# Performance work log

Hardware: AMD Instinct MI355X
Metric: run time of the kernel (lower is better)

Reference implementation:

```python
import jax, jax.numpy as jnp
import numpy as np

N, E, H, HEADS, L, B = 16000, 256000, 192, 4, 4, 8
C = H // HEADS
VN, VE, T = 32, 8, 1000


def _sin_emb(t, dim):
    half = dim // 2
    freqs = jnp.exp(-np.log(10000.0) * jnp.arange(half, dtype=jnp.float32) / half)
    ang = t.astype(jnp.float32)[:, None] * freqs[None, :]
    return jnp.concatenate([jnp.sin(ang), jnp.cos(ang)], axis=-1)


def _ln(x, g, b, eps=1e-5):
    mu = jnp.mean(x, -1, keepdims=True)
    var = jnp.mean(jnp.square(x - mu), -1, keepdims=True)
    return (x - mu) * jax.lax.rsqrt(var + eps) * g + b


def setup_inputs():
    key = jax.random.key(0)
    ks = iter(jax.random.split(key, 64))
    p = lambda shape, s=0.02: jax.random.normal(next(ks), shape, jnp.float32) * s
    inp = {}
    inp['node_emb'] = p((VN, H))
    inp['edge_emb'] = p((VE, H))
    inp['time_w1'] = p((H, H)); inp['time_b1'] = jnp.zeros((H,), jnp.float32)
    inp['time_w2'] = p((H, H)); inp['time_b2'] = jnp.zeros((H,), jnp.float32)
    inp['mask_emb'] = p((2, H))
    inp['wq'] = p((L, H, H)); inp['bq'] = jnp.zeros((L, H), jnp.float32)
    inp['wk'] = p((L, H, H)); inp['bk'] = jnp.zeros((L, H), jnp.float32)
    inp['wv'] = p((L, H, H)); inp['bv'] = jnp.zeros((L, H), jnp.float32)
    inp['we'] = p((L, H, H))
    inp['wskip'] = p((L, H, H)); inp['bskip'] = jnp.zeros((L, H), jnp.float32)
    inp['wbeta'] = p((L, 3 * H))
    inp['ln_g'] = jnp.ones((L, H), jnp.float32); inp['ln_b'] = jnp.zeros((L, H), jnp.float32)
    inp['node_out_w'] = p((H, VN)); inp['node_out_b'] = jnp.zeros((VN,), jnp.float32)
    inp['edge_w1'] = p((4 * H, H)); inp['edge_b1'] = jnp.zeros((H,), jnp.float32)
    inp['edge_w2'] = p((H, VE)); inp['edge_b2'] = jnp.zeros((VE,), jnp.float32)
    inp['node_type'] = jax.random.randint(next(ks), (N,), 0, VN)
    inp['edge_type'] = jax.random.randint(next(ks), (E,), 0, VE)
    inp['edge_index'] = jax.random.randint(next(ks), (2, E), 0, N)
    inp['edit_mask'] = jax.random.randint(next(ks), (N,), 0, 2, dtype=jnp.int32)
    inp['node_batch'] = jnp.sort(jax.random.randint(next(ks), (N,), 0, B))
    inp['t_graph'] = jax.random.randint(next(ks), (B,), 1, T)
    return inp


def reference(node_emb, edge_emb, time_w1, time_b1, time_w2, time_b2, mask_emb,
              wq, bq, wk, bk, wv, bv, we, wskip, bskip, wbeta, ln_g, ln_b,
              node_out_w, node_out_b, edge_w1, edge_b1, edge_w2, edge_b2,
              node_type, edge_type, edge_index, edit_mask, node_batch, t_graph):
    src, dst = edge_index[0], edge_index[1]
    # time embedding: sinusoidal -> Linear -> SiLU -> Linear  => [B, H]
    t_vec = jax.nn.silu(_sin_emb(t_graph, H) @ time_w1 + time_b1) @ time_w2 + time_b2
    t_node = t_vec[node_batch]              # [N, H]
    t_edge = t_vec[node_batch[src]]         # [E, H]
    x = node_emb[node_type] + t_node + mask_emb[edit_mask]
    edge_attr = edge_emb[edge_type] + t_edge
    scale = 1.0 / np.sqrt(C)
    for l in range(L):
        q = (x @ wq[l] + bq[l]).reshape(N, HEADS, C)
        k = (x @ wk[l] + bk[l]).reshape(N, HEADS, C)
        v = (x @ wv[l] + bv[l]).reshape(N, HEADS, C)
        e = (edge_attr @ we[l]).reshape(E, HEADS, C)
        kj = k[src] + e                                   # [E, heads, C]
        score = jnp.sum(q[dst] * kj, axis=-1) * scale      # [E, heads]
        m = jax.ops.segment_max(score, dst, num_segments=N)
        ex = jnp.exp(score - m[dst])
        denom = jax.ops.segment_sum(ex, dst, num_segments=N)
        alpha = ex / denom[dst]
        msg = (v[src] + e) * alpha[..., None]              # [E, heads, C]
        out = jax.ops.segment_sum(msg, dst, num_segments=N).reshape(N, H)
        xr = x @ wskip[l] + bskip[l]
        beta = jax.nn.sigmoid(jnp.concatenate([out, xr, out - xr], -1) @ wbeta[l])[:, None]
        h = beta * xr + (1.0 - beta) * out
        x = _ln(x + h, ln_g[l], ln_b[l])
    node_logits = x @ node_out_w + node_out_b
    edge_feat = jnp.concatenate([x[src], x[dst], edge_attr, t_edge], -1)  # [E, 4H]
    edge_logits = jax.nn.silu(edge_feat @ edge_w1 + edge_b1) @ edge_w2 + edge_b2
    return node_logits, edge_logits
```

## Files before the change

### kernel.cpp

```cpp
#include <hip/hip_runtime.h>
#include <hip/hip_bf16.h>
#include <math.h>

#define NN 16000
#define NPAD 16128
#define NE 256000
#define H 192
#define RP 256
#define NL 4
#define NBATCH 8
#define VEt 8
#define HH (H*H)
#define EML 16

typedef __hip_bfloat16 bf16;
typedef unsigned short u16;
typedef unsigned char u8;
typedef unsigned int u32;
typedef __attribute__((ext_vector_type(8))) short bfrag_t;
typedef __attribute__((ext_vector_type(4))) float facc_t;
typedef __attribute__((ext_vector_type(4))) float f4;

__device__ __forceinline__ bf16 f2b(float v){ return __float2bfloat16(v); }

__device__ __forceinline__ unsigned enc8sw(float x){
    unsigned u = __float_as_uint(x);
    unsigned s = (u >> 24) & 0x80u;
    float ax = fabsf(x);
    if(ax >= 448.f) return s | 0x7Eu;
    if(ax < 0.015625f){
        int q = (int)rintf(ax * 512.f);
        return s | (unsigned)q;
    }
    unsigned au = u & 0x7FFFFFFFu;
    unsigned lsb = (au >> 20) & 1u;
    au += 0x7FFFFu + lsb;
    unsigned E = (au >> 23) - 127u;
    unsigned M = (au >> 20) & 7u;
    if((int)E > 8) return s | 0x7Eu;
    return s | ((E + 7u) << 3) | M;
}
__device__ __forceinline__ unsigned enc8(float x){
#if __has_builtin(__builtin_amdgcn_cvt_pk_fp8_f32)
    return (u32)__builtin_amdgcn_cvt_pk_fp8_f32(x, x, 0, false) & 0xFFu;
#else
    return enc8sw(x);
#endif
}
template<int SEL>
__device__ __forceinline__ float dec8s(u32 w){
#if __has_builtin(__builtin_amdgcn_cvt_f32_fp8)
    return __builtin_amdgcn_cvt_f32_fp8((int)w, SEL);
#else
    unsigned v = (w >> (SEL*8)) & 0xFFu;
    unsigned e = (v >> 3) & 15u, m = v & 7u;
    float mag = e ? __builtin_ldexpf((float)(8u + m), (int)e - 10)
                  : __builtin_ldexpf((float)m, -9);
    return (v & 0x80u) ? -mag : mag;
#endif
}
__device__ __forceinline__ float frcp(float x){
#if __has_builtin(__builtin_amdgcn_rcpf)
    return __builtin_amdgcn_rcpf(x);
#else
    return 1.f/x;
#endif
}

__global__ void k_sentinel(float* __restrict__ out, float v){ out[0] = v; }

__global__ void k_transpose(const float* __restrict__ wq, const float* __restrict__ wk,
                            const float* __restrict__ wv, const float* __restrict__ wsk,
                            const float* __restrict__ w1, u16* __restrict__ wt){
    int mat = blockIdx.x;
    const float* src;
    if(mat < 4)       src = wq  + (size_t)mat*HH;
    else if(mat < 8)  src = wk  + (size_t)(mat-4)*HH;
    else if(mat < 12) src = wv  + (size_t)(mat-8)*HH;
    else if(mat < 16) src = wsk + (size_t)(mat-12)*HH;
    else              src = w1  + (size_t)(mat-16)*HH;
    u16* dst = wt + (size_t)mat*HH;
    const int slice = HH/8;
    int base = blockIdx.y*slice;
    for(int i = base + threadIdx.x; i < base + slice; i += blockDim.x){
        int k = i / H, n = i % H;
        bf16 b = f2b(src[i]);
        dst[n*H + k] = *(u16*)&b;
    }
}

__global__ void k_tvec(const int* __restrict__ tg, const float* __restrict__ w1,
                       const float* __restrict__ b1, const float* __restrict__ w2,
                       const float* __restrict__ b2, float* __restrict__ tvec){
    int b = blockIdx.x, j = threadIdx.x;
    __shared__ float emb[H], h1[H];
    float t = (float)tg[b];
    if(j < 96){
        float fr = __expf(-logf(10000.0f) * (float)j / 96.0f);
        float ang = t * fr;
        emb[j]      = sinf(ang);
        emb[j + 96] = cosf(ang);
    }
    __syncthreads();
    float acc = b1[j];
    for(int k = 0; k < H; k++) acc += emb[k] * w1[k*H + j];
    h1[j] = acc / (1.f + __expf(-acc));
    __syncthreads();
    float acc2 = b2[j];
    for(int k = 0; k < H; k++) acc2 += h1[k] * w2[k*H + j];
    tvec[b*H + j] = acc2;
}

__global__ void k_init_x(const float* __restrict__ nemb, const float* __restrict__ memb,
                         const float* __restrict__ tvec, const int* __restrict__ ntype,
                         const int* __restrict__ emask, const int* __restrict__ nbatch,
                         float* __restrict__ x, u16* __restrict__ xb){
    int idx = blockIdx.x*blockDim.x + threadIdx.x;
    if(idx >= NN*H) return;
    int n = idx / H, c = idx % H;
    float v = nemb[(size_t)ntype[n]*H + c] + tvec[nbatch[n]*H + c]
            + memb[(size_t)emask[n]*H + c];
    x[idx] = v;
    bf16 b = f2b(v); xb[idx] = *(u16*)&b;
}

__global__ void k_zero_i(int* __restrict__ p, int n){
    int i = blockIdx.x*blockDim.x + threadIdx.x;
    if(i < n) p[i] = 0;
}
__global__ void k_count(const int* __restrict__ edst, int* __restrict__ cnt){
    int e = blockIdx.x*blockDim.x + threadIdx.x;
    if(e < NE) atomicAdd(&cnt[edst[e]], 1);
}
__global__ __launch_bounds__(1024) void k_scan(const int* __restrict__ cnt,
                                               int* __restrict__ ofs, int* __restrict__ cur){
    __shared__ int wsum[16];
    __shared__ int carry_s;
    int tid = threadIdx.x, lane = tid & 63, w = tid >> 6;
    if(tid == 0) carry_s = 0;
    __syncthreads();
    for(int base = 0; base < NN; base += 1024){
        int idx = base + tid;
        int v = (idx < NN) ? cnt[idx] : 0;
        int sc = v;
        #pragma unroll
        for(int o = 1; o < 64; o <<= 1){
            int t = __shfl_up(sc, o);
            if(lane >= o) sc += t;
        }
        if(lane == 63) wsum[w] = sc;
        __syncthreads();
        if(w == 0){
            int ws = (lane < 16) ? wsum[lane] : 0;
            #pragma unroll
            for(int o = 1; o < 16; o <<= 1){
                int t = __shfl_up(ws, o);
                if(lane >= o) ws += t;
            }
            if(lane < 16) wsum[lane] = ws;
        }
        __syncthreads();
        int wbase = (w > 0) ? wsum[w-1] : 0;
        int c = carry_s;
        int excl = c + wbase + sc - v;
        if(idx < NN){ ofs[idx] = excl; cur[idx] = excl; }
        __syncthreads();
        if(tid == 0) carry_s = c + wsum[15];
        __syncthreads();
    }
    if(threadIdx.x == 0) ofs[NN] = carry_s;
}
__global__ void k_scatter(const int* __restrict__ esrc, const int* __restrict__ edst,
                          const int* __restrict__ etype, const int* __restrict__ nbatch,
                          int* __restrict__ cur, int* __restrict__ ssrc, int* __restrict__ seix){
    int e = blockIdx.x*blockDim.x + threadIdx.x;
    if(e >= NE) return;
    int s = esrc[e], d = edst[e];
    int pos = atomicAdd(&cur[d], 1);
    ssrc[pos] = s;
    seix[pos] = nbatch[s]*VEt + etype[e];
}

__global__ void k_etab(const float* __restrict__ eemb, const float* __restrict__ tvec,
                       const float* __restrict__ we, float* __restrict__ etab){
    int blk = blockIdx.x;
    int l = blk >> 6, idx = blk & 63, b = idx >> 3, et = idx & 7;
    int c = threadIdx.x;
    __shared__ float a[H];
    a[c] = eemb[et*H + c] + tvec[b*H + c];
    __syncthreads();
    float acc = 0.f;
    const float* w = we + (size_t)l*HH;
    for(int k = 0; k < H; k++) acc += a[k] * w[k*H + c];
    etab[(size_t)blk*RP + (c/3)*4 + (c%3)] = acc;
}

__global__ void k_ctab(const float* __restrict__ eemb, const float* __restrict__ tvec,
                       const float* __restrict__ w1, const float* __restrict__ b1,
                       float* __restrict__ ctab){
    int idx = blockIdx.x, b = idx >> 3, et = idx & 7;
    int c = threadIdx.x;
    __shared__ float a[H];
    a[c] = eemb[et*H + c] + tvec[b*H + c];
    __syncthreads();
    float acc = b1[c];
    for(int k = 0; k < H; k++){
        acc += a[k]          * w1[(size_t)(2*H + k)*H + c];
        acc += tvec[b*H + k] * w1[(size_t)(3*H + k)*H + c];
    }
    ctab[(size_t)idx*RP + (c/3)*4 + (c%3)] = acc;
}

struct GemmP {
    const u16* wt[4];
    const float* bias[4];
    void* out[4];
    int obf[4];
};
__global__ __launch_bounds__(256) void k_gemm(const u16* __restrict__ A, GemmP P){
    int oi = blockIdx.y / 3, nt = blockIdx.y % 3;
    const u16* Wt = P.wt[oi];
    const float* bias = P.bias[oi];
    int wave = threadIdx.x >> 6, lane = threadIdx.x & 63;
    int quad = lane >> 4, l16 = lane & 15;
    int m0 = blockIdx.x*256 + wave*64;
    int n0 = nt*64;
    facc_t acc[4][4];
    #pragma unroll
    for(int i = 0; i < 4; i++)
        #pragma unroll
        for(int j = 0; j < 4; j++){ acc[i][j][0]=0.f; acc[i][j][1]=0.f; acc[i][j][2]=0.f; acc[i][j][3]=0.f; }
    #pragma unroll
    for(int kc = 0; kc < 6; kc++){
        int kb = kc*32 + quad*8;
        bfrag_t af[4], bg[4];
        #pragma unroll
        for(int i = 0; i < 4; i++) af[i] = *(const bfrag_t*)(A  + (size_t)(m0 + i*16 + l16)*H + kb);
        #pragma unroll
        for(int j = 0; j < 4; j++) bg[j] = *(const bfrag_t*)(Wt + (size_t)(n0 + j*16 + l16)*H + kb);
        #pragma unroll
        for(int i = 0; i < 4; i++)
            #pragma unroll
            for(int j = 0; j < 4; j++)
                acc[i][j] = __builtin_amdgcn_mfma_f32_16x16x32_bf16(af[i], bg[j], acc[i][j], 0, 0, 0);
    }
    float bv[4];
    #pragma unroll
    for(int j = 0; j < 4; j++) bv[j] = bias ? bias[n0 + j*16 + l16] : 0.f;
    if(P.obf[oi] == 2){
        u8* out = (u8*)P.out[oi];
        int byteoff[4];
        #pragma unroll
        for(int j = 0; j < 4; j++){
            int c = n0 + j*16 + l16;
            byteoff[j] = (c/3)*4 + (c%3);
        }
        #pragma unroll
        for(int i = 0; i < 4; i++){
            int rb = m0 + i*16 + quad*4;
            #pragma unroll
            for(int r = 0; r < 4; r++){
                int row = rb + r;
                if(row < NN){
                    #pragma unroll
                    for(int j = 0; j < 4; j++)
                        out[(size_t)row*RP + byteoff[j]] = (u8)enc8(acc[i][j][r] + bv[j]);
                }
            }
        }
    } else {
        float* out = (float*)P.out[oi];
        #pragma unroll
        for(int i = 0; i < 4; i++){
            int rb = m0 + i*16 + quad*4;
            #pragma unroll
            for(int r = 0; r < 4; r++){
                int row = rb + r;
                if(row < NN){
                    #pragma unroll
                    for(int j = 0; j < 4; j++)
                        out[(size_t)row*H + n0 + j*16 + l16] = acc[i][j][r] + bv[j];
                }
            }
        }
    }
}

__global__ __launch_bounds__(256) void k_attn(
    const float* __restrict__ Q, const u8* __restrict__ Kb,
    const u8* __restrict__ Vb, const float* __restrict__ XR,
    const float* __restrict__ etab, const int* __restrict__ ofs,
    const int* __restrict__ ssrc, const int* __restrict__ seix,
    const float* __restrict__ wb, const float* __restrict__ lng, const float* __restrict__ lnb,
    float* __restrict__ x, u16* __restrict__ xb)
{
    int n = blockIdx.x*4 + (threadIdx.x >> 6);
    int lane = threadIdx.x & 63;
    int ch = lane*3;
    size_t base = (size_t)n*H + ch;
    const float scale = 0.14433756729740646f;
    float q0 = Q[base], q1 = Q[base+1], q2 = Q[base+2];
    int p0 = ofs[n], p1 = ofs[n+1];
    float lac[4]  = {0.f,0.f,0.f,0.f};
    float ac0[4]  = {0.f,0.f,0.f,0.f};
    float ac1[4]  = {0.f,0.f,0.f,0.f};
    float ac2[4]  = {0.f,0.f,0.f,0.f};
    int p = p0;
    for(; p + 3 < p1; p += 4){
        int s[4], ei[4];
        #pragma unroll
        for(int t = 0; t < 4; t++){ s[t] = ssrc[p+t]; ei[t] = seix[p+t]; }
        u32 kw[4], vw[4];
        f4 ef[4];
        #pragma unroll
        for(int t = 0; t < 4; t++){
            kw[t] = *(const u32*)(Kb + (size_t)s[t]*RP + lane*4);
            ef[t] = *(const f4*)(etab + (size_t)ei[t]*RP + lane*4);
            vw[t] = *(const u32*)(Vb + (size_t)s[t]*RP + lane*4);
        }
        float tt[4];
        #pragma unroll
        for(int t = 0; t < 4; t++)
            tt[t] = q0*(dec8s<0>(kw[t])+ef[t].x) + q1*(dec8s<1>(kw[t])+ef[t].y)
                  + q2*(dec8s<2>(kw[t])+ef[t].z);
        #pragma unroll
        for(int o = 1; o <= 8; o <<= 1){
            #pragma unroll
            for(int t = 0; t < 4; t++) tt[t] += __shfl_xor(tt[t], o);
        }
        #pragma unroll
        for(int t = 0; t < 4; t++){
            float sc = fminf(fmaxf(tt[t]*scale, -60.f), 60.f);
            float pw = __expf(sc);
            lac[t] += pw;
            ac0[t] += pw*(dec8s<0>(vw[t])+ef[t].x);
            ac1[t] += pw*(dec8s<1>(vw[t])+ef[t].y);
            ac2[t] += pw*(dec8s<2>(vw[t])+ef[t].z);
        }
    }
    for(; p < p1; p++){
        int sA = ssrc[p], eiA = seix[p];
        u32 kwA = *(const u32*)(Kb + (size_t)sA*RP + lane*4);
        f4 efA = *(const f4*)(etab + (size_t)eiA*RP + lane*4);
        u32 vwA = *(const u32*)(Vb + (size_t)sA*RP + lane*4);
        float tA = q0*(dec8s<0>(kwA)+efA.x) + q1*(dec8s<1>(kwA)+efA.y) + q2*(dec8s<2>(kwA)+efA.z);
        tA += __shfl_xor(tA,1); tA += __shfl_xor(tA,2); tA += __shfl_xor(tA,4); tA += __shfl_xor(tA,8);
        float sc = fminf(fmaxf(tA*scale, -60.f), 60.f);
        float pw = __expf(sc);
        lac[0] += pw;
        ac0[0] += pw*(dec8s<0>(vwA)+efA.x);
        ac1[0] += pw*(dec8s<1>(vwA)+efA.y);
        ac2[0] += pw*(dec8s<2>(vwA)+efA.z);
    }
    float l  = (lac[0]+lac[1]) + (lac[2]+lac[3]);
    float a0 = (ac0[0]+ac0[1]) + (ac0[2]+ac0[3]);
    float a1 = (ac1[0]+ac1[1]) + (ac1[2]+ac1[3]);
    float a2 = (ac2[0]+ac2[1]) + (ac2[2]+ac2[3]);
    float inv = (p1 > p0) ? 1.f/l : 0.f;
    float o0 = a0*inv, o1 = a1*inv, o2 = a2*inv;
    float xr0 = XR[base], xr1 = XR[base+1], xr2 = XR[base+2];
    float sd = o0*wb[ch]  + o1*wb[ch+1]  + o2*wb[ch+2]
             + xr0*wb[H+ch] + xr1*wb[H+ch+1] + xr2*wb[H+ch+2]
             + (o0-xr0)*wb[2*H+ch] + (o1-xr1)*wb[2*H+ch+1] + (o2-xr2)*wb[2*H+ch+2];
    sd += __shfl_xor(sd,1); sd += __shfl_xor(sd,2); sd += __shfl_xor(sd,4);
    sd += __shfl_xor(sd,8); sd += __shfl_xor(sd,16); sd += __shfl_xor(sd,32);
    float beta = 1.f/(1.f + __expf(-sd));
    float h0 = beta*xr0 + (1.f-beta)*o0;
    float h1 = beta*xr1 + (1.f-beta)*o1;
    float h2 = beta*xr2 + (1.f-beta)*o2;
    float y0 = x[base] + h0, y1 = x[base+1] + h1, y2 = x[base+2] + h2;
    float s3 = y0 + y1 + y2;
    s3 += __shfl_xor(s3,1); s3 += __shfl_xor(s3,2); s3 += __shfl_xor(s3,4);
    s3 += __shfl_xor(s3,8); s3 += __shfl_xor(s3,16); s3 += __shfl_xor(s3,32);
    float mean = s3 * (1.f/H);
    float d0 = y0-mean, d1 = y1-mean, d2 = y2-mean;
    float v3 = d0*d0 + d1*d1 + d2*d2;
    v3 += __shfl_xor(v3,1); v3 += __shfl_xor(v3,2); v3 += __shfl_xor(v3,4);
    v3 += __shfl_xor(v3,8); v3 += __shfl_xor(v3,16); v3 += __shfl_xor(v3,32);
    float rs = rsqrtf(v3*(1.f/H) + 1e-5f);
    float z0 = d0*rs*lng[ch]   + lnb[ch];
    float z1 = d1*rs*lng[ch+1] + lnb[ch+1];
    float z2 = d2*rs*lng[ch+2] + lnb[ch+2];
    x[base] = z0; x[base+1] = z1; x[base+2] = z2;
    bf16 t0 = f2b(z0), t1 = f2b(z1), t2 = f2b(z2);
    xb[base] = *(u16*)&t0; xb[base+1] = *(u16*)&t1; xb[base+2] = *(u16*)&t2;
}

__global__ void k_nodeout(const float* __restrict__ x, const float* __restrict__ w,
                          const float* __restrict__ b, float* __restrict__ out){
    int j = threadIdx.x & 31;
    int n = blockIdx.x*8 + (threadIdx.x >> 5);
    float acc = b[j];
    const float* xr = x + (size_t)n*H;
    for(int k = 0; k < H; k++) acc += xr[k] * w[k*32 + j];
    out[(size_t)n*32 + j] = acc;
}

__global__ __launch_bounds__(256) void k_edgemlp(
    const int* __restrict__ esrc, const int* __restrict__ edst, const int* __restrict__ etype,
    const int* __restrict__ nb,
    const u8* __restrict__ xs1, const u8* __restrict__ xd1, const float* __restrict__ ctab,
    const float* __restrict__ w2, const float* __restrict__ b2p, float* __restrict__ out)
{
    int wid = blockIdx.x*4 + (threadIdx.x >> 6);
    int lane = threadIdx.x & 63;
    int ch = lane*3;
    float w2r[3][8];
    #pragma unroll
    for(int t = 0; t < 3; t++)
        #pragma unroll
        for(int j = 0; j < 8; j++) w2r[t][j] = w2[(ch+t)*8 + j];
    int jout = (lane&1)*4 + (lane&2) + ((lane&4)>>2);
    float bo = (lane < 8) ? b2p[jout] : 0.f;
    int b0 = lane & 1, b1 = lane & 2, b2m = lane & 4;
    int e0 = wid*EML;
    for(int eb = e0; eb < e0 + EML; eb += 2){
        int sX = esrc[eb],   dX = edst[eb];
        int sY = esrc[eb+1], dY = edst[eb+1];
        int ctX = nb[sX]*VEt + etype[eb];
        int ctY = nb[sY]*VEt + etype[eb+1];
        u32 awX = *(const u32*)(xs1 + (size_t)sX*RP + lane*4);
        u32 awY = *(const u32*)(xs1 + (size_t)sY*RP + lane*4);
        u32 bwX = *(const u32*)(xd1 + (size_t)dX*RP + lane*4);
        u32 bwY = *(const u32*)(xd1 + (size_t)dY*RP + lane*4);
        f4  cfX = *(const f4*)(ctab + (size_t)ctX*RP + lane*4);
        f4  cfY = *(const f4*)(ctab + (size_t)ctY*RP + lane*4);
        float hX0, hX1, hX2, hY0, hY1, hY2;
        { float v = dec8s<0>(awX)+dec8s<0>(bwX)+cfX.x; hX0 = v*frcp(1.f+__expf(-v)); }
        { float v = dec8s<1>(awX)+dec8s<1>(bwX)+cfX.y; hX1 = v*frcp(1.f+__expf(-v)); }
        { float v = dec8s<2>(awX)+dec8s<2>(bwX)+cfX.z; hX2 = v*frcp(1.f+__expf(-v)); }
        { float v = dec8s<0>(awY)+dec8s<0>(bwY)+cfY.x; hY0 = v*frcp(1.f+__expf(-v)); }
        { float v = dec8s<1>(awY)+dec8s<1>(bwY)+cfY.y; hY1 = v*frcp(1.f+__expf(-v)); }
        { float v = dec8s<2>(awY)+dec8s<2>(bwY)+cfY.z; hY2 = v*frcp(1.f+__expf(-v)); }
        float pjX[8], pjY[8];
        #pragma unroll
        for(int j = 0; j < 8; j++){
            pjX[j] = hX0*w2r[0][j] + hX1*w2r[1][j] + hX2*w2r[2][j];
            pjY[j] = hY0*w2r[0][j] + hY1*w2r[1][j] + hY2*w2r[2][j];
        }
        float v4X[4], v4Y[4];
        #pragma unroll
        for(int t = 0; t < 4; t++){
            float sX4 = b0 ? pjX[t] : pjX[t+4];
            float kX4 = b0 ? pjX[t+4] : pjX[t];
            v4X[t] = kX4 + __shfl_xor(sX4, 1);
            float sY4 = b0 ? pjY[t] : pjY[t+4];
            float kY4 = b0 ? pjY[t+4] : pjY[t];
            v4Y[t] = kY4 + __shfl_xor(sY4, 1);
        }
        float v2X[2], v2Y[2];
        #pragma unroll
        for(int t = 0; t < 2; t++){
            float sX2 = b1 ? v4X[t] : v4X[t+2];
            float kX2 = b1 ? v4X[t+2] : v4X[t];
            v2X[t] = kX2 + __shfl_xor(sX2, 2);
            float sY2 = b1 ? v4Y[t] : v4Y[t+2];
            float kY2 = b1 ? v4Y[t+2] : v4Y[t];
            v2Y[t] = kY2 + __shfl_xor(sY2, 2);
        }
        float v1X, v1Y;
        {
            float sX1 = b2m ? v2X[0] : v2X[1];
            float kX1 = b2m ? v2X[1] : v2X[0];
            v1X = kX1 + __shfl_xor(sX1, 4);
            float sY1 = b2m ? v2Y[0] : v2Y[1];
            float kY1 = b2m ? v2Y[1] : v2Y[0];
            v1Y = kY1 + __shfl_xor(sY1, 4);
        }
        v1X += __shfl_xor(v1X, 8);  v1Y += __shfl_xor(v1Y, 8);
        v1X += __shfl_xor(v1X, 16); v1Y += __shfl_xor(v1Y, 16);
        v1X += __shfl_xor(v1X, 32); v1Y += __shfl_xor(v1Y, 32);
        if(lane < 8){
            out[(size_t)eb*8 + jout]     = v1X + bo;
            out[(size_t)(eb+1)*8 + jout] = v1Y + bo;
        }
    }
}

extern "C" void kernel_launch(void* const* d_in, const int* in_sizes, int n_in,
                              void* d_out, int out_size, void* d_ws, size_t ws_size,
                              hipStream_t stream)
{
    {
        int bad = -1;
        if(n_in != 31) bad = 100;
        else {
            const int chk_idx[9] = {0, 7, 16, 21, 23, 26, 27, 29, 30};
            const int chk_sz [9] = {32*H, NL*HH, NL*3*H, 4*HH, H*8, NE, 2*NE, NN, NBATCH};
            for(int i = 0; i < 9; i++) if(in_sizes[chk_idx[i]] != chk_sz[i]){ bad = chk_idx[i]; break; }
        }
        if(bad >= 0){ k_sentinel<<<1,1,0,stream>>>((float*)d_out, 20000.f + 256.f*bad); return; }
        if(out_size != NN*32 + NE*8){ k_sentinel<<<1,1,0,stream>>>((float*)d_out, 30000.f); return; }
    }

    const float* node_emb = (const float*)d_in[0];
    const float* edge_emb = (const float*)d_in[1];
    const float* time_w1  = (const float*)d_in[2];
    const float* time_b1  = (const float*)d_in[3];
    const float* time_w2  = (const float*)d_in[4];
    const float* time_b2  = (const float*)d_in[5];
    const float* mask_emb = (const float*)d_in[6];
    const float* wq       = (const float*)d_in[7];
    const float* bq       = (const float*)d_in[8];
    const float* wk       = (const float*)d_in[9];
    const float* bk       = (const float*)d_in[10];
    const float* wv       = (const float*)d_in[11];
    const float* bv       = (const float*)d_in[12];
    const float* we       = (const float*)d_in[13];
    const float* wskip    = (const float*)d_in[14];
    const float* bskip    = (const float*)d_in[15];
    const float* wbeta    = (const float*)d_in[16];
    const float* ln_g     = (const float*)d_in[17];
    const float* ln_b     = (const float*)d_in[18];
    const float* now      = (const float*)d_in[19];
    const float* nob      = (const float*)d_in[20];
    const float* ew1      = (const float*)d_in[21];
    const float* eb1      = (const float*)d_in[22];
    const float* ew2      = (const float*)d_in[23];
    const float* eb2      = (const float*)d_in[24];
    const int* node_type  = (const int*)d_in[25];
    const int* edge_type  = (const int*)d_in[26];
    const int* edge_index = (const int*)d_in[27];
    const int* edit_mask  = (const int*)d_in[28];
    const int* node_batch = (const int*)d_in[29];
    const int* t_graph    = (const int*)d_in[30];
    const int* esrc = edge_index;
    const int* edst = edge_index + NE;

    char* wsb = (char*)d_ws;
    size_t off = 0;
    auto take = [&](size_t bytes) -> char* {
        char* r = wsb + off;
        off += (bytes + 255) & ~(size_t)255;
        return r;
    };
    float* tvec = (float*)take((size_t)NBATCH*H*4);
    float* x    = (float*)take((size_t)NN*H*4);
    u16*   xb   = (u16*)  take((size_t)NPAD*H*2);
    float* Q    = (float*)take((size_t)NN*H*4);
    u8*    Kb   = (u8*)   take((size_t)NN*RP);
    u8*    Vb   = (u8*)   take((size_t)NN*RP);
    float* XR   = (float*)take((size_t)NN*H*4);
    u8*    xs1  = (u8*)   take((size_t)NN*RP);
    u8*    xd1  = (u8*)   take((size_t)NN*RP);
    float* etab = (float*)take((size_t)NL*64*RP*4);
    float* ctab = (float*)take((size_t)64*RP*4);
    u16*   wt   = (u16*)  take((size_t)18*HH*2);
    int* cnt    = (int*)  take((size_t)(NN+1)*4);
    int* offa   = (int*)  take((size_t)(NN+1)*4);
    int* cur    = (int*)  take((size_t)(NN+1)*4);
    int* ssrc   = (int*)  take((size_t)NE*4);
    int* seix   = (int*)  take((size_t)NE*4);

    if(ws_size < off){
        k_sentinel<<<1,1,0,stream>>>((float*)d_out, 10000.f + (float)(ws_size >> 20));
        return;
    }

    k_transpose<<<dim3(18, 8), 256, 0, stream>>>(wq, wk, wv, wskip, ew1, wt);
    k_tvec<<<NBATCH, H, 0, stream>>>(t_graph, time_w1, time_b1, time_w2, time_b2, tvec);
    k_init_x<<<(NN*H + 255)/256, 256, 0, stream>>>(node_emb, mask_emb, tvec, node_type,
                                                   edit_mask, node_batch, x, xb);
    k_zero_i<<<(NN + 255)/256, 256, 0, stream>>>(cnt, NN);
    k_count<<<NE/256, 256, 0, stream>>>(edst, cnt);
    k_scan<<<1, 1024, 0, stream>>>(cnt, offa, cur);
    k_scatter<<<NE/256, 256, 0, stream>>>(esrc, edst, edge_type, node_batch, cur, ssrc, seix);
    k_etab<<<NL*64, H, 0, stream>>>(edge_emb, tvec, we, etab);
    k_ctab<<<64, H, 0, stream>>>(edge_emb, tvec, ew1, eb1, ctab);

    for(int l = 0; l < NL; l++){
        GemmP P;
        P.wt[0] = wt + (size_t)(0  + l)*HH;  P.bias[0] = bq   + (size_t)l*H;  P.out[0] = Q;  P.obf[0] = 0;
        P.wt[1] = wt + (size_t)(4  + l)*HH;  P.bias[1] = bk   + (size_t)l*H;  P.out[1] = Kb; P.obf[1] = 2;
        P.wt[2] = wt + (size_t)(8  + l)*HH;  P.bias[2] = bv   + (size_t)l*H;  P.out[2] = Vb; P.obf[2] = 2;
        P.wt[3] = wt + (size_t)(12 + l)*HH;  P.bias[3] = bskip+ (size_t)l*H;  P.out[3] = XR; P.obf[3] = 0;
        k_gemm<<<dim3(63, 12), 256, 0, stream>>>(xb, P);
        k_attn<<<NN/4, 256, 0, stream>>>(Q, Kb, Vb, XR, etab + (size_t)l*64*RP, offa, ssrc, seix,
                                         wbeta + (size_t)l*3*H, ln_g + (size_t)l*H,
                                         ln_b + (size_t)l*H, x, xb);
    }
    {
        GemmP P;
        P.wt[0] = wt + (size_t)16*HH; P.bias[0] = nullptr; P.out[0] = xs1; P.obf[0] = 2;
        P.wt[1] = wt + (size_t)17*HH; P.bias[1] = nullptr; P.out[1] = xd1; P.obf[1] = 2;
        P.wt[2] = P.wt[0]; P.bias[2] = nullptr; P.out[2] = xs1; P.obf[2] = 2;
        P.wt[3] = P.wt[0]; P.bias[3] = nullptr; P.out[3] = xs1; P.obf[3] = 2;
        k_gemm<<<dim3(63, 6), 256, 0, stream>>>(xb, P);
    }
    k_nodeout<<<NN/8, 256, 0, stream>>>(x, now, nob, (float*)d_out);
    k_edgemlp<<<NE/(4*EML), 256, 0, stream>>>(esrc, edst, edge_type, node_batch, xs1, xd1, ctab,
                                              ew2, eb2, (float*)d_out + (size_t)NN*32);
}
```

Measured before the change: 552.1 us.

## Interleave K/V fp8 rows and run edge MLP second layer on MFMA

K and V fp8 outputs of the projection GEMM are stored interleaved in one 512-byte row per node, so the attention kernel fetches both with a single 8-byte gather per edge instead of two 4-byte gathers. The edge MLP is restructured so each wave handles 16 edges with lanes mapped to MFMA fragments. It computes SiLU of the gathered hidden features, packs them to bf16 and multiplies by a pre-transposed, zero-padded W2 with 16x16x32 MFMA, replacing the shuffle-reduction tree. The xs1/xd1/ctab layouts become dense 192-wide rows, and bf16 rounding of the hidden activation adds some precision loss.

```diff
diff --git a/kernel.cpp b/kernel.cpp
--- a/kernel.cpp
+++ b/kernel.cpp
@@ -11,7 +11,6 @@
 #define NBATCH 8
 #define VEt 8
 #define HH (H*H)
-#define EML 16
 
 typedef __hip_bfloat16 bf16;
 typedef unsigned short u16;
@@ -20,8 +19,10 @@
 typedef __attribute__((ext_vector_type(8))) short bfrag_t;
 typedef __attribute__((ext_vector_type(4))) float facc_t;
 typedef __attribute__((ext_vector_type(4))) float f4;
+typedef __attribute__((ext_vector_type(2))) unsigned uv2;
 
 __device__ __forceinline__ bf16 f2b(float v){ return __float2bfloat16(v); }
+__device__ __forceinline__ short f2bs(float v){ bf16 b = __float2bfloat16(v); return *(short*)&b; }
 
 __device__ __forceinline__ unsigned enc8sw(float x){
     unsigned u = __float_as_uint(x);
@@ -66,6 +67,7 @@
     return 1.f/x;
 #endif
 }
+__device__ __forceinline__ float fsilu(float v){ return v*frcp(1.f + __expf(-v)); }
 
 __global__ void k_sentinel(float* __restrict__ out, float v){ out[0] = v; }
 
@@ -89,6 +91,14 @@
     }
 }
 
+__global__ void k_w2t(const float* __restrict__ w2, u16* __restrict__ w2t){
+    for(int i = threadIdx.x; i < 16*H; i += blockDim.x){
+        int n = i / H, k = i % H;
+        bf16 b = f2b(n < 8 ? w2[k*8 + n] : 0.f);
+        w2t[i] = *(u16*)&b;
+    }
+}
+
 __global__ void k_tvec(const int* __restrict__ tg, const float* __restrict__ w1,
                        const float* __restrict__ b1, const float* __restrict__ w2,
                        const float* __restrict__ b2, float* __restrict__ tvec){
@@ -208,7 +218,7 @@
         acc += a[k]          * w1[(size_t)(2*H + k)*H + c];
         acc += tvec[b*H + k] * w1[(size_t)(3*H + k)*H + c];
     }
-    ctab[(size_t)idx*RP + (c/3)*4 + (c%3)] = acc;
+    ctab[(size_t)idx*H + c] = acc;
 }
 
 struct GemmP {
@@ -247,28 +257,8 @@
     float bv[4];
     #pragma unroll
     for(int j = 0; j < 4; j++) bv[j] = bias ? bias[n0 + j*16 + l16] : 0.f;
-    if(P.obf[oi] == 2){
-        u8* out = (u8*)P.out[oi];
-        int byteoff[4];
-        #pragma unroll
-        for(int j = 0; j < 4; j++){
-            int c = n0 + j*16 + l16;
-            byteoff[j] = (c/3)*4 + (c%3);
-        }
-        #pragma unroll
-        for(int i = 0; i < 4; i++){
-            int rb = m0 + i*16 + quad*4;
-            #pragma unroll
-            for(int r = 0; r < 4; r++){
-                int row = rb + r;
-                if(row < NN){
-                    #pragma unroll
-                    for(int j = 0; j < 4; j++)
-                        out[(size_t)row*RP + byteoff[j]] = (u8)enc8(acc[i][j][r] + bv[j]);
-                }
-            }
-        }
-    } else {
+    int code = P.obf[oi];
+    if(code == 0){
         float* out = (float*)P.out[oi];
         #pragma unroll
         for(int i = 0; i < 4; i++){
@@ -283,12 +273,36 @@
                 }
             }
         }
+    } else {
+        u8* out = (u8*)P.out[oi];
+        int rstride = (code == 4) ? 192 : 512;
+        int byteoff[4];
+        #pragma unroll
+        for(int j = 0; j < 4; j++){
+            int c = n0 + j*16 + l16;
+            if(code == 4)      byteoff[j] = c;
+            else if(code == 2) byteoff[j] = (c/3)*8 + (c%3);
+            else               byteoff[j] = (c/3)*8 + 4 + (c%3);
+        }
+        #pragma unroll
+        for(int i = 0; i < 4; i++){
+            int rb = m0 + i*16 + quad*4;
+            #pragma unroll
+            for(int r = 0; r < 4; r++){
+                int row = rb + r;
+                if(row < NN){
+                    #pragma unroll
+                    for(int j = 0; j < 4; j++)
+                        out[(size_t)row*rstride + byteoff[j]] = (u8)enc8(acc[i][j][r] + bv[j]);
+                }
+            }
+        }
     }
 }
 
 __global__ __launch_bounds__(256) void k_attn(
-    const float* __restrict__ Q, const u8* __restrict__ Kb,
-    const u8* __restrict__ Vb, const float* __restrict__ XR,
+    const float* __restrict__ Q, const u8* __restrict__ KV,
+    const float* __restrict__ XR,
     const float* __restrict__ etab, const int* __restrict__ ofs,
     const int* __restrict__ ssrc, const int* __restrict__ seix,
     const float* __restrict__ wb, const float* __restrict__ lng, const float* __restrict__ lnb,
@@ -310,19 +324,18 @@
         int s[4], ei[4];
         #pragma unroll
         for(int t = 0; t < 4; t++){ s[t] = ssrc[p+t]; ei[t] = seix[p+t]; }
-        u32 kw[4], vw[4];
+        uv2 kv[4];
         f4 ef[4];
         #pragma unroll
         for(int t = 0; t < 4; t++){
-            kw[t] = *(const u32*)(Kb + (size_t)s[t]*RP + lane*4);
+            kv[t] = *(const uv2*)(KV + (size_t)s[t]*512 + lane*8);
             ef[t] = *(const f4*)(etab + (size_t)ei[t]*RP + lane*4);
-            vw[t] = *(const u32*)(Vb + (size_t)s[t]*RP + lane*4);
         }
         float tt[4];
         #pragma unroll
         for(int t = 0; t < 4; t++)
-            tt[t] = q0*(dec8s<0>(kw[t])+ef[t].x) + q1*(dec8s<1>(kw[t])+ef[t].y)
-                  + q2*(dec8s<2>(kw[t])+ef[t].z);
+            tt[t] = q0*(dec8s<0>(kv[t].x)+ef[t].x) + q1*(dec8s<1>(kv[t].x)+ef[t].y)
+                  + q2*(dec8s<2>(kv[t].x)+ef[t].z);
         #pragma unroll
         for(int o = 1; o <= 8; o <<= 1){
             #pragma unroll
@@ -333,24 +346,23 @@
             float sc = fminf(fmaxf(tt[t]*scale, -60.f), 60.f);
             float pw = __expf(sc);
             lac[t] += pw;
-            ac0[t] += pw*(dec8s<0>(vw[t])+ef[t].x);
-            ac1[t] += pw*(dec8s<1>(vw[t])+ef[t].y);
-            ac2[t] += pw*(dec8s<2>(vw[t])+ef[t].z);
+            ac0[t] += pw*(dec8s<0>(kv[t].y)+ef[t].x);
+            ac1[t] += pw*(dec8s<1>(kv[t].y)+ef[t].y);
+            ac2[t] += pw*(dec8s<2>(kv[t].y)+ef[t].z);
         }
     }
     for(; p < p1; p++){
         int sA = ssrc[p], eiA = seix[p];
-        u32 kwA = *(const u32*)(Kb + (size_t)sA*RP + lane*4);
+        uv2 kv = *(const uv2*)(KV + (size_t)sA*512 + lane*8);
         f4 efA = *(const f4*)(etab + (size_t)eiA*RP + lane*4);
-        u32 vwA = *(const u32*)(Vb + (size_t)sA*RP + lane*4);
-        float tA = q0*(dec8s<0>(kwA)+efA.x) + q1*(dec8s<1>(kwA)+efA.y) + q2*(dec8s<2>(kwA)+efA.z);
+        float tA = q0*(dec8s<0>(kv.x)+efA.x) + q1*(dec8s<1>(kv.x)+efA.y) + q2*(dec8s<2>(kv.x)+efA.z);
         tA += __shfl_xor(tA,1); tA += __shfl_xor(tA,2); tA += __shfl_xor(tA,4); tA += __shfl_xor(tA,8);
         float sc = fminf(fmaxf(tA*scale, -60.f), 60.f);
         float pw = __expf(sc);
         lac[0] += pw;
-        ac0[0] += pw*(dec8s<0>(vwA)+efA.x);
-        ac1[0] += pw*(dec8s<1>(vwA)+efA.y);
-        ac2[0] += pw*(dec8s<2>(vwA)+efA.z);
+        ac0[0] += pw*(dec8s<0>(kv.y)+efA.x);
+        ac1[0] += pw*(dec8s<1>(kv.y)+efA.y);
+        ac2[0] += pw*(dec8s<2>(kv.y)+efA.z);
     }
     float l  = (lac[0]+lac[1]) + (lac[2]+lac[3]);
     float a0 = (ac0[0]+ac0[1]) + (ac0[2]+ac0[3]);
@@ -400,79 +412,46 @@
     const int* __restrict__ esrc, const int* __restrict__ edst, const int* __restrict__ etype,
     const int* __restrict__ nb,
     const u8* __restrict__ xs1, const u8* __restrict__ xd1, const float* __restrict__ ctab,
-    const float* __restrict__ w2, const float* __restrict__ b2p, float* __restrict__ out)
+    const u16* __restrict__ w2t, const float* __restrict__ b2p, float* __restrict__ out)
 {
     int wid = blockIdx.x*4 + (threadIdx.x >> 6);
     int lane = threadIdx.x & 63;
-    int ch = lane*3;
-    float w2r[3][8];
+    int l16 = lane & 15, quad = lane >> 4;
+    int e0 = wid*16;
+    int e = e0 + l16;
+    int s = esrc[e], d = edst[e];
+    int ct = nb[s]*VEt + etype[e];
+    const u8* ap = xs1 + (size_t)s*192;
+    const u8* bp = xd1 + (size_t)d*192;
+    const float* cp = ctab + (size_t)ct*H;
+    facc_t acc = {0.f, 0.f, 0.f, 0.f};
     #pragma unroll
-    for(int t = 0; t < 3; t++)
-        #pragma unroll
-        for(int j = 0; j < 8; j++) w2r[t][j] = w2[(ch+t)*8 + j];
-    int jout = (lane&1)*4 + (lane&2) + ((lane&4)>>2);
-    float bo = (lane < 8) ? b2p[jout] : 0.f;
-    int b0 = lane & 1, b1 = lane & 2, b2m = lane & 4;
-    int e0 = wid*EML;
-    for(int eb = e0; eb < e0 + EML; eb += 2){
-        int sX = esrc[eb],   dX = edst[eb];
-        int sY = esrc[eb+1], dY = edst[eb+1];
-        int ctX = nb[sX]*VEt + etype[eb];
-        int ctY = nb[sY]*VEt + etype[eb+1];
-        u32 awX = *(const u32*)(xs1 + (size_t)sX*RP + lane*4);
-        u32 awY = *(const u32*)(xs1 + (size_t)sY*RP + lane*4);
-        u32 bwX = *(const u32*)(xd1 + (size_t)dX*RP + lane*4);
-        u32 bwY = *(const u32*)(xd1 + (size_t)dY*RP + lane*4);
-        f4  cfX = *(const f4*)(ctab + (size_t)ctX*RP + lane*4);
-        f4  cfY = *(const f4*)(ctab + (size_t)ctY*RP + lane*4);
-        float hX0, hX1, hX2, hY0, hY1, hY2;
-        { float v = dec8s<0>(awX)+dec8s<0>(bwX)+cfX.x; hX0 = v*frcp(1.f+__expf(-v)); }
-        { float v = dec8s<1>(awX)+dec8s<1>(bwX)+cfX.y; hX1 = v*frcp(1.f+__expf(-v)); }
-        { float v = dec8s<2>(awX)+dec8s<2>(bwX)+cfX.z; hX2 = v*frcp(1.f+__expf(-v)); }
-        { float v = dec8s<0>(awY)+dec8s<0>(bwY)+cfY.x; hY0 = v*frcp(1.f+__expf(-v)); }
-        { float v = dec8s<1>(awY)+dec8s<1>(bwY)+cfY.y; hY1 = v*frcp(1.f+__expf(-v)); }
-        { float v = dec8s<2>(awY)+dec8s<2>(bwY)+cfY.z; hY2 = v*frcp(1.f+__expf(-v)); }
-        float pjX[8], pjY[8];
-        #pragma unroll
-        for(int j = 0; j < 8; j++){
-            pjX[j] = hX0*w2r[0][j] + hX1*w2r[1][j] + hX2*w2r[2][j];
-            pjY[j] = hY0*w2r[0][j] + hY1*w2r[1][j] + hY2*w2r[2][j];
-        }
-        float v4X[4], v4Y[4];
-        #pragma unroll
-        for(int t = 0; t < 4; t++){
-            float sX4 = b0 ? pjX[t] : pjX[t+4];
-            float kX4 = b0 ? pjX[t+4] : pjX[t];
-            v4X[t] = kX4 + __shfl_xor(sX4, 1);
-            float sY4 = b0 ? pjY[t] : pjY[t+4];
-            float kY4 = b0 ? pjY[t+4] : pjY[t];
-            v4Y[t] = kY4 + __shfl_xor(sY4, 1);
-        }
-        float v2X[2], v2Y[2];
-        #pragma unroll
-        for(int t = 0; t < 2; t++){
-            float sX2 = b1 ? v4X[t] : v4X[t+2];
-            float kX2 = b1 ? v4X[t+2] : v4X[t];
-            v2X[t] = kX2 + __shfl_xor(sX2, 2);
-            float sY2 = b1 ? v4Y[t] : v4Y[t+2];
-            float kY2 = b1 ? v4Y[t+2] : v4Y[t];
-            v2Y[t] = kY2 + __shfl_xor(sY2, 2);
-        }
-        float v1X, v1Y;
-        {
-            float sX1 = b2m ? v2X[0] : v2X[1];
-            float kX1 = b2m ? v2X[1] : v2X[0];
-            v1X = kX1 + __shfl_xor(sX1, 4);
-            float sY1 = b2m ? v2Y[0] : v2Y[1];
-            float kY1 = b2m ? v2Y[1] : v2Y[0];
-            v1Y = kY1 + __shfl_xor(sY1, 4);
-        }
-        v1X += __shfl_xor(v1X, 8);  v1Y += __shfl_xor(v1Y, 8);
-        v1X += __shfl_xor(v1X, 16); v1Y += __shfl_xor(v1Y, 16);
-        v1X += __shfl_xor(v1X, 32); v1Y += __shfl_xor(v1Y, 32);
-        if(lane < 8){
-            out[(size_t)eb*8 + jout]     = v1X + bo;
-            out[(size_t)(eb+1)*8 + jout] = v1Y + bo;
+    for(int kc = 0; kc < 6; kc++){
+        int kb = quad*8 + kc*32;
+        u32 aw0 = *(const u32*)(ap + kb), aw1 = *(const u32*)(ap + kb + 4);
+        u32 bw0 = *(const u32*)(bp + kb), bw1 = *(const u32*)(bp + kb + 4);
+        f4 c0 = *(const f4*)(cp + kb);
+        f4 c1 = *(const f4*)(cp + kb + 4);
+        float h0 = fsilu(dec8s<0>(aw0) + dec8s<0>(bw0) + c0.x);
+        float h1 = fsilu(dec8s<1>(aw0) + dec8s<1>(bw0) + c0.y);
+        float h2 = fsilu(dec8s<2>(aw0) + dec8s<2>(bw0) + c0.z);
+        float h3 = fsilu(dec8s<3>(aw0) + dec8s<3>(bw0) + c0.w);
+        float h4 = fsilu(dec8s<0>(aw1) + dec8s<0>(bw1) + c1.x);
+        float h5 = fsilu(dec8s<1>(aw1) + dec8s<1>(bw1) + c1.y);
+        float h6 = fsilu(dec8s<2>(aw1) + dec8s<2>(bw1) + c1.z);
+        float h7 = fsilu(dec8s<3>(aw1) + dec8s<3>(bw1) + c1.w);
+        bfrag_t af;
+        af[0] = f2bs(h0); af[1] = f2bs(h1); af[2] = f2bs(h2); af[3] = f2bs(h3);
+        af[4] = f2bs(h4); af[5] = f2bs(h5); af[6] = f2bs(h6); af[7] = f2bs(h7);
+        bfrag_t wf = *(const bfrag_t*)(w2t + (size_t)l16*H + kb);
+        acc = __builtin_amdgcn_mfma_f32_16x16x32_bf16(af, wf, acc, 0, 0, 0);
+    }
+    if(l16 < 8){
+        float bo = b2p[l16];
+        #pragma unroll
+        for(int r = 0; r < 4; r++){
+            int eo = e0 + quad*4 + r;
+            out[(size_t)eo*8 + l16] = acc[r] + bo;
         }
     }
 }
@@ -538,14 +517,14 @@
     float* x    = (float*)take((size_t)NN*H*4);
     u16*   xb   = (u16*)  take((size_t)NPAD*H*2);
     float* Q    = (float*)take((size_t)NN*H*4);
-    u8*    Kb   = (u8*)   take((size_t)NN*RP);
-    u8*    Vb   = (u8*)   take((size_t)NN*RP);
+    u8*    KV   = (u8*)   take((size_t)NN*512);
     float* XR   = (float*)take((size_t)NN*H*4);
-    u8*    xs1  = (u8*)   take((size_t)NN*RP);
-    u8*    xd1  = (u8*)   take((size_t)NN*RP);
+    u8*    xs1  = (u8*)   take((size_t)NN*192);
+    u8*    xd1  = (u8*)   take((size_t)NN*192);
     float* etab = (float*)take((size_t)NL*64*RP*4);
-    float* ctab = (float*)take((size_t)64*RP*4);
+    float* ctab = (float*)take((size_t)64*H*4);
     u16*   wt   = (u16*)  take((size_t)18*HH*2);
+    u16*   w2t  = (u16*)  take((size_t)16*H*2);
     int* cnt    = (int*)  take((size_t)(NN+1)*4);
     int* offa   = (int*)  take((size_t)(NN+1)*4);
     int* cur    = (int*)  take((size_t)(NN+1)*4);
@@ -558,6 +537,7 @@
     }
 
     k_transpose<<<dim3(18, 8), 256, 0, stream>>>(wq, wk, wv, wskip, ew1, wt);
+    k_w2t<<<1, 256, 0, stream>>>(ew2, w2t);
     k_tvec<<<NBATCH, H, 0, stream>>>(t_graph, time_w1, time_b1, time_w2, time_b2, tvec);
     k_init_x<<<(NN*H + 255)/256, 256, 0, stream>>>(node_emb, mask_emb, tvec, node_type,
                                                    edit_mask, node_batch, x, xb);
@@ -571,23 +551,23 @@
     for(int l = 0; l < NL; l++){
         GemmP P;
         P.wt[0] = wt + (size_t)(0  + l)*HH;  P.bias[0] = bq   + (size_t)l*H;  P.out[0] = Q;  P.obf[0] = 0;
-        P.wt[1] = wt + (size_t)(4  + l)*HH;  P.bias[1] = bk   + (size_t)l*H;  P.out[1] = Kb; P.obf[1] = 2;
-        P.wt[2] = wt + (size_t)(8  + l)*HH;  P.bias[2] = bv   + (size_t)l*H;  P.out[2] = Vb; P.obf[2] = 2;
+        P.wt[1] = wt + (size_t)(4  + l)*HH;  P.bias[1] = bk   + (size_t)l*H;  P.out[1] = KV; P.obf[1] = 2;
+        P.wt[2] = wt + (size_t)(8  + l)*HH;  P.bias[2] = bv   + (size_t)l*H;  P.out[2] = KV; P.obf[2] = 3;
         P.wt[3] = wt + (size_t)(12 + l)*HH;  P.bias[3] = bskip+ (size_t)l*H;  P.out[3] = XR; P.obf[3] = 0;
         k_gemm<<<dim3(63, 12), 256, 0, stream>>>(xb, P);
-        k_attn<<<NN/4, 256, 0, stream>>>(Q, Kb, Vb, XR, etab + (size_t)l*64*RP, offa, ssrc, seix,
+        k_attn<<<NN/4, 256, 0, stream>>>(Q, KV, XR, etab + (size_t)l*64*RP, offa, ssrc, seix,
                                          wbeta + (size_t)l*3*H, ln_g + (size_t)l*H,
                                          ln_b + (size_t)l*H, x, xb);
     }
     {
         GemmP P;
-        P.wt[0] = wt + (size_t)16*HH; P.bias[0] = nullptr; P.out[0] = xs1; P.obf[0] = 2;
-        P.wt[1] = wt + (size_t)17*HH; P.bias[1] = nullptr; P.out[1] = xd1; P.obf[1] = 2;
-        P.wt[2] = P.wt[0]; P.bias[2] = nullptr; P.out[2] = xs1; P.obf[2] = 2;
-        P.wt[3] = P.wt[0]; P.bias[3] = nullptr; P.out[3] = xs1; P.obf[3] = 2;
+        P.wt[0] = wt + (size_t)16*HH; P.bias[0] = nullptr; P.out[0] = xs1; P.obf[0] = 4;
+        P.wt[1] = wt + (size_t)17*HH; P.bias[1] = nullptr; P.out[1] = xd1; P.obf[1] = 4;
+        P.wt[2] = P.wt[0]; P.bias[2] = nullptr; P.out[2] = xs1; P.obf[2] = 4;
+        P.wt[3] = P.wt[0]; P.bias[3] = nullptr; P.out[3] = xs1; P.obf[3] = 4;
         k_gemm<<<dim3(63, 6), 256, 0, stream>>>(xb, P);
     }
     k_nodeout<<<NN/8, 256, 0, stream>>>(x, now, nob, (float*)d_out);
-    k_edgemlp<<<NE/(4*EML), 256, 0, stream>>>(esrc, edst, edge_type, node_batch, xs1, xd1, ctab,
-                                              ew2, eb2, (float*)d_out + (size_t)NN*32);
-}
+    k_edgemlp<<<NE/64, 256, 0, stream>>>(esrc, edst, edge_type, node_batch, xs1, xd1, ctab,
+                                         w2t, eb2, (float*)d_out + (size_t)NN*32);
+}
```

Result: no change. 561.7 us (+1.7%).
